# Optimization experiments

Hardware: AMD Instinct MI355X
Metric: run time of the kernel (lower is better)

Reference implementation:

```python
import jax, jax.numpy as jnp
import numpy as np

H = 1024   # hidden_size == memory_size
NH = 4     # num_attention_heads
HD = H // NH
M = 8192   # total memory items
B, S = 4, 2048
EPS = 1e-5


def _ln(x, g, b):
    mu = jnp.mean(x, -1, keepdims=True)
    var = jnp.mean((x - mu) ** 2, -1, keepdims=True)
    return (x - mu) / jnp.sqrt(var + EPS) * g + b


def setup_inputs() -> dict:
    key = jax.random.key(0)
    ks = jax.random.split(key, 16)
    s = 0.02
    return {
        "query_hidden": jax.random.normal(ks[0], (B, S, H), jnp.float32),
        "mem_keys": jax.random.normal(ks[1], (M, H), jnp.float32),
        "importance": jax.random.uniform(ks[2], (M,), jnp.float32),
        "recency": jax.random.uniform(ks[3], (M,), jnp.float32),
        "access_count": jax.random.uniform(ks[4], (M,), jnp.float32),
        "Wq": s * jax.random.normal(ks[5], (H, H), jnp.float32),
        "bq": jnp.zeros((H,), jnp.float32),
        "in_w": s * jax.random.normal(ks[6], (3 * H, H), jnp.float32),
        "in_b": jnp.zeros((3 * H,), jnp.float32),
        "out_w": s * jax.random.normal(ks[7], (H, H), jnp.float32),
        "out_b": jnp.zeros((H,), jnp.float32),
        "gate_w": s * jax.random.normal(ks[8], (H, 2 * H), jnp.float32),
        "gate_b": jnp.zeros((H,), jnp.float32),
        "int_w1": s * jax.random.normal(ks[9], (2 * H, 2 * H), jnp.float32),
        "int_b1": jnp.zeros((2 * H,), jnp.float32),
        "int_ln_g": jnp.ones((2 * H,), jnp.float32),
        "int_ln_b": jnp.zeros((2 * H,), jnp.float32),
        "int_w2": s * jax.random.normal(ks[10], (H, 2 * H), jnp.float32),
        "int_b2": jnp.zeros((H,), jnp.float32),
        "ln1_g": jnp.ones((H,), jnp.float32),
        "ln1_b": jnp.zeros((H,), jnp.float32),
        "ln2_g": jnp.ones((H,), jnp.float32),
        "ln2_b": jnp.zeros((H,), jnp.float32),
        "sel_params": jnp.ones((3,), jnp.float32) / 3.0,
        "top_k": 2048,
    }


def reference(query_hidden, mem_keys, importance, recency, access_count,
              Wq, bq, in_w, in_b, out_w, out_b, gate_w, gate_b,
              int_w1, int_b1, int_ln_g, int_ln_b, int_w2, int_b2,
              ln1_g, ln1_b, ln2_g, ln2_b, sel_params, top_k):
    b, s, _ = query_hidden.shape
    # HTPS selection: softmax-weighted mix of importance / recency / frequency
    w = jax.nn.softmax(sel_params)
    freq = access_count / jnp.max(access_count)
    sel = w[0] * importance + w[1] * recency + w[2] * freq
    _, idx = jax.lax.top_k(sel, top_k)
    mem = mem_keys[idx]                      # [K, H]
    mem_n = _ln(mem, ln1_g, ln1_b)           # layer_norm1 on memory

    q = query_hidden @ Wq.T + bq             # query_proj  [B,S,H]
    wq, wk, wv = in_w[:H], in_w[H:2 * H], in_w[2 * H:]
    bqi, bki, bvi = in_b[:H], in_b[H:2 * H], in_b[2 * H:]
    # Batched MHA: the per-position loop is equivalent to all S queries at once
    Q = (q @ wq.T + bqi).reshape(b, s, NH, HD)
    K = (mem_n @ wk.T + bki).reshape(top_k, NH, HD)   # shared across batch
    V = (mem_n @ wv.T + bvi).reshape(top_k, NH, HD)
    scores = jnp.einsum('bshd,khd->bhsk', Q, K) / jnp.sqrt(jnp.float32(HD))
    attn = jax.nn.softmax(scores, axis=-1)
    ctx = jnp.einsum('bhsk,khd->bshd', attn, V).reshape(b, s, H)
    attn_out = ctx @ out_w.T + out_b

    cat = jnp.concatenate([query_hidden, attn_out], axis=-1)   # [B,S,2H]
    gate = jax.nn.sigmoid(cat @ gate_w.T + gate_b)
    h1 = _ln(cat @ int_w1.T + int_b1, int_ln_g, int_ln_b)
    integ = jax.nn.gelu(h1, approximate=False) @ int_w2.T + int_b2
    return _ln(query_hidden + gate * integ, ln2_g, ln2_b)
```

## Files before the change

kernel.cpp:

```cpp
#include <hip/hip_runtime.h>

#define HDIM 1024
#define MMEM 8192
#define TOPK 2048
#define NROWS 8192
#define LNEPS 1e-5f

typedef unsigned short ushort_t;
typedef __bf16 bf16x8 __attribute__((ext_vector_type(8)));
typedef float f32x4 __attribute__((ext_vector_type(4)));
typedef __attribute__((address_space(1))) const void GVoid;
typedef __attribute__((address_space(3))) void LVoid;

__device__ __forceinline__ ushort_t f2bf(float f) {
    union { float f; unsigned u; } c; c.f = f;
    unsigned r = c.u + 0x7fffu + ((c.u >> 16) & 1u);
    return (ushort_t)(r >> 16);
}
__device__ __forceinline__ float bf2f(ushort_t u) {
    union { unsigned u; float f; } c; c.u = ((unsigned)u) << 16; return c.f;
}
__device__ __forceinline__ float blk_red(float v, int op, float* red) {
    #pragma unroll
    for (int o = 32; o; o >>= 1) {
        float u = __shfl_down(v, o);
        v = op ? fmaxf(v, u) : v + u;
    }
    if ((threadIdx.x & 63) == 0) red[threadIdx.x >> 6] = v;
    __syncthreads();
    float r = op ? fmaxf(fmaxf(red[0], red[1]), fmaxf(red[2], red[3]))
                 : (red[0] + red[1]) + (red[2] + red[3]);
    __syncthreads();
    return r;
}

__global__ __launch_bounds__(256) void sel_prep(const float* __restrict__ sp,
        const float* __restrict__ imp, const float* __restrict__ rec,
        const float* __restrict__ ac, float* __restrict__ sel) {
    __shared__ float red[4];
    float p0 = sp[0], p1 = sp[1], p2 = sp[2];
    float mx = fmaxf(p0, fmaxf(p1, p2));
    float e0 = expf(p0 - mx), e1 = expf(p1 - mx), e2 = expf(p2 - mx);
    float inv = 1.f / (e0 + e1 + e2);
    float w0 = e0 * inv, w1 = e1 * inv, w2 = e2 * inv;
    float m = -1e30f;
    for (int i = threadIdx.x; i < MMEM; i += 256) m = fmaxf(m, ac[i]);
    m = blk_red(m, 1, red);
    float rinv = 1.f / m;
    for (int i = threadIdx.x; i < MMEM; i += 256)
        sel[i] = w0 * imp[i] + w1 * rec[i] + w2 * (ac[i] * rinv);
}

__global__ __launch_bounds__(256) void topk_rank(const float* __restrict__ sel,
                                                 int* __restrict__ idx) {
    __shared__ float s[MMEM];
    __shared__ int pc[256];
    for (int t = threadIdx.x; t < MMEM / 4; t += 256)
        reinterpret_cast<float4*>(s)[t] = reinterpret_cast<const float4*>(sel)[t];
    __syncthreads();
    const int li = threadIdx.x & 31;
    const int jc = threadIdx.x >> 5;
    const int i  = blockIdx.x * 32 + li;
    const float si = s[i];
    int cnt = 0;
    const float4* sv = reinterpret_cast<const float4*>(s) + jc * 256;
    #pragma unroll 4
    for (int t = 0; t < 256; ++t) {
        float4 v = sv[t];
        int j0 = jc * 1024 + t * 4;
        cnt += (v.x > si) || (v.x == si && (j0 + 0) < i);
        cnt += (v.y > si) || (v.y == si && (j0 + 1) < i);
        cnt += (v.z > si) || (v.z == si && (j0 + 2) < i);
        cnt += (v.w > si) || (v.w == si && (j0 + 3) < i);
    }
    pc[threadIdx.x] = cnt;
    __syncthreads();
    if (threadIdx.x < 32) {
        int r = 0;
        #pragma unroll
        for (int c = 0; c < 8; ++c) r += pc[c * 32 + threadIdx.x];
        if (r < TOPK) idx[r] = blockIdx.x * 32 + threadIdx.x;
    }
}

__global__ __launch_bounds__(256) void gather_ln(const float* __restrict__ mem_keys,
        const int* __restrict__ idx, const float* __restrict__ g,
        const float* __restrict__ b, ushort_t* __restrict__ out) {
    __shared__ float red[4];
    int src = idx[blockIdx.x] & (MMEM - 1);
    const float* x = mem_keys + (size_t)src * HDIM;
    float4 v = reinterpret_cast<const float4*>(x)[threadIdx.x];
    float s = v.x + v.y + v.z + v.w;
    float ss = v.x*v.x + v.y*v.y + v.z*v.z + v.w*v.w;
    s  = blk_red(s, 0, red);
    ss = blk_red(ss, 0, red);
    float mu = s * (1.f / HDIM);
    float var = ss * (1.f / HDIM) - mu * mu;
    float rstd = rsqrtf(var + LNEPS);
    int c = threadIdx.x * 4;
    ushort4 o;
    o.x = f2bf((v.x - mu) * rstd * g[c+0] + b[c+0]);
    o.y = f2bf((v.y - mu) * rstd * g[c+1] + b[c+1]);
    o.z = f2bf((v.z - mu) * rstd * g[c+2] + b[c+2]);
    o.w = f2bf((v.w - mu) * rstd * g[c+3] + b[c+3]);
    *reinterpret_cast<ushort4*>(out + (size_t)blockIdx.x * HDIM + c) = o;
}

__global__ __launch_bounds__(256) void cvt_bf16(const float* __restrict__ in,
                                                ushort_t* __restrict__ out) {
    size_t i = ((size_t)blockIdx.x * 256 + threadIdx.x) * 4;
    float4 v = *reinterpret_cast<const float4*>(in + i);
    ushort4 o = { f2bf(v.x), f2bf(v.y), f2bf(v.z), f2bf(v.w) };
    *reinterpret_cast<ushort4*>(out + i) = o;
}

__global__ __launch_bounds__(256) void cvt_t_bf16(const float* __restrict__ in,
                                                  ushort_t* __restrict__ out) {
    __shared__ ushort_t t[64][65];
    const int bx = blockIdx.x * 64, by = blockIdx.y * 64;
    const int r = threadIdx.x >> 4, c4 = (threadIdx.x & 15) << 2;
    #pragma unroll
    for (int rr = 0; rr < 64; rr += 16) {
        float4 v = *reinterpret_cast<const float4*>(in + (size_t)(by + r + rr) * 1024 + bx + c4);
        t[r + rr][c4 + 0] = f2bf(v.x);
        t[r + rr][c4 + 1] = f2bf(v.y);
        t[r + rr][c4 + 2] = f2bf(v.z);
        t[r + rr][c4 + 3] = f2bf(v.w);
    }
    __syncthreads();
    #pragma unroll
    for (int rr = 0; rr < 64; rr += 16) {
        const int i = r + rr;
        ushort4 o = { t[c4 + 0][i], t[c4 + 1][i], t[c4 + 2][i], t[c4 + 3][i] };
        *reinterpret_cast<ushort4*>(out + (size_t)(bx + i) * 1024 + by + c4) = o;
    }
}

__global__ __launch_bounds__(256) void bias_fold(const float* __restrict__ wq,
        const float* __restrict__ bq, const float* __restrict__ bqi,
        float* __restrict__ beff) {
    __shared__ float red[4];
    const float4 wv = reinterpret_cast<const float4*>(wq + (size_t)blockIdx.x * 1024)[threadIdx.x];
    const float4 bv = reinterpret_cast<const float4*>(bq)[threadIdx.x];
    float s = wv.x*bv.x + wv.y*bv.y + wv.z*bv.z + wv.w*bv.w;
    s = blk_red(s, 0, red);
    if (threadIdx.x == 0) beff[blockIdx.x] = s + bqi[blockIdx.x];
}

__global__ __launch_bounds__(256) void cvt_x_cat(const float* __restrict__ x,
                                                 ushort_t* __restrict__ cat) {
    size_t i = ((size_t)blockIdx.x * 256 + threadIdx.x) * 4;
    size_t row = i >> 10, col = i & 1023;
    float4 v = *reinterpret_cast<const float4*>(x + i);
    ushort4 o = { f2bf(v.x), f2bf(v.y), f2bf(v.z), f2bf(v.w) };
    *reinterpret_cast<ushort4*>(cat + row * 2048 + col) = o;
}

__global__ __launch_bounds__(256) void softmax_rows(ushort_t* __restrict__ sc) {
    __shared__ float red[4];
    ushort_t* p = sc + (size_t)blockIdx.x * 2048 + threadIdx.x * 8;
    ushort4 a = reinterpret_cast<const ushort4*>(p)[0];
    ushort4 bq = reinterpret_cast<const ushort4*>(p)[1];
    float v[8] = { bf2f(a.x), bf2f(a.y), bf2f(a.z), bf2f(a.w),
                   bf2f(bq.x), bf2f(bq.y), bf2f(bq.z), bf2f(bq.w) };
    float mx = v[0];
    #pragma unroll
    for (int j = 1; j < 8; ++j) mx = fmaxf(mx, v[j]);
    mx = blk_red(mx, 1, red);
    float s = 0.f;
    #pragma unroll
    for (int j = 0; j < 8; ++j) { v[j] = expf(v[j] - mx); s += v[j]; }
    s = blk_red(s, 0, red);
    float inv = 1.f / s;
    ushort4 o1 = { f2bf(v[0]*inv), f2bf(v[1]*inv), f2bf(v[2]*inv), f2bf(v[3]*inv) };
    ushort4 o2 = { f2bf(v[4]*inv), f2bf(v[5]*inv), f2bf(v[6]*inv), f2bf(v[7]*inv) };
    reinterpret_cast<ushort4*>(p)[0] = o1;
    reinterpret_cast<ushort4*>(p)[1] = o2;
}

__global__ __launch_bounds__(256) void ln_gelu(ushort_t* h1,
        const float* __restrict__ g, const float* __restrict__ b) {
    __shared__ float red[4];
    ushort_t* p = h1 + (size_t)blockIdx.x * 2048 + threadIdx.x * 8;
    ushort4 a = reinterpret_cast<const ushort4*>(p)[0];
    ushort4 c = reinterpret_cast<const ushort4*>(p)[1];
    float v[8] = { bf2f(a.x), bf2f(a.y), bf2f(a.z), bf2f(a.w),
                   bf2f(c.x), bf2f(c.y), bf2f(c.z), bf2f(c.w) };
    float s = 0.f, ss = 0.f;
    #pragma unroll
    for (int j = 0; j < 8; ++j) { s += v[j]; ss += v[j]*v[j]; }
    s  = blk_red(s, 0, red);
    ss = blk_red(ss, 0, red);
    float mu = s * (1.f / 2048.f);
    float var = ss * (1.f / 2048.f) - mu * mu;
    float rstd = rsqrtf(var + LNEPS);
    int c0 = threadIdx.x * 8;
    ushort_t o[8];
    #pragma unroll
    for (int j = 0; j < 8; ++j) {
        float xn = (v[j] - mu) * rstd * g[c0 + j] + b[c0 + j];
        float ge = 0.5f * xn * (1.f + erff(xn * 0.70710678118654752f));
        o[j] = f2bf(ge);
    }
    ushort4 o1 = { o[0], o[1], o[2], o[3] };
    ushort4 o2 = { o[4], o[5], o[6], o[7] };
    reinterpret_cast<ushort4*>(p)[0] = o1;
    reinterpret_cast<ushort4*>(p)[1] = o2;
}

__global__ __launch_bounds__(256) void final_ln(const float* __restrict__ x,
        const float* gate, const ushort_t* __restrict__ integ,
        const float* __restrict__ g, const float* __restrict__ b,
        float* out) {
    __shared__ float red[4];
    size_t base = (size_t)blockIdx.x * HDIM + threadIdx.x * 4;
    float4 xv = *reinterpret_cast<const float4*>(x + base);
    float4 gv = *reinterpret_cast<const float4*>(gate + base);
    ushort4 iv = *reinterpret_cast<const ushort4*>(integ + base);
    float v[4] = { xv.x + gv.x*bf2f(iv.x), xv.y + gv.y*bf2f(iv.y),
                   xv.z + gv.z*bf2f(iv.z), xv.w + gv.w*bf2f(iv.w) };
    float s = v[0]+v[1]+v[2]+v[3];
    float ss = v[0]*v[0]+v[1]*v[1]+v[2]*v[2]+v[3]*v[3];
    s  = blk_red(s, 0, red);
    ss = blk_red(ss, 0, red);
    float mu = s * (1.f / HDIM);
    float var = ss * (1.f / HDIM) - mu * mu;
    float rstd = rsqrtf(var + LNEPS);
    int c = threadIdx.x * 4;
    float4 o;
    o.x = (v[0] - mu) * rstd * g[c+0] + b[c+0];
    o.y = (v[1] - mu) * rstd * g[c+1] + b[c+1];
    o.z = (v[2] - mu) * rstd * g[c+2] + b[c+2];
    o.w = (v[3] - mu) * rstd * g[c+3] + b[c+3];
    *reinterpret_cast<float4*>(out + base) = o;
}

template<int EPI, int BIAS>
__global__ __launch_bounds__(256, 2)
void gemm_bt(const ushort_t* __restrict__ A, const ushort_t* __restrict__ B,
             const float* __restrict__ bias, void* __restrict__ Cv,
             int K, int lda, int ldb, int ldc,
             long long sA1, long long sA2, long long sAz,
             long long sB1, long long sB2, long long sBz,
             long long sC1, long long sC2, long long sCz,
             int z2n, int zbase, float scale)
{
    __shared__ __align__(16) ushort_t As[8192];
    __shared__ __align__(16) ushort_t Bs[8192];
    const int zz = blockIdx.z;
    const int zg = zz + zbase;
    const int z1 = zg / z2n, z2 = zg - z1 * z2n;
    A += (size_t)(z1 * sA1 + z2 * sA2 + zz * sAz);
    B += (size_t)(z1 * sB1 + z2 * sB2 + zz * sBz);
    const size_t cOff = (size_t)(z1 * sC1 + z2 * sC2 + zz * sCz);

    const int nwg = gridDim.x * gridDim.y;
    const int wg  = blockIdx.y * gridDim.x + blockIdx.x;
    const int q8  = nwg >> 3, r8 = nwg & 7;
    const int xcd = wg & 7, lo = wg >> 3;
    const int wgid = (xcd < r8 ? xcd * (q8 + 1) : r8 * (q8 + 1) + (xcd - r8) * q8) + lo;
    const int m0 = (wgid / gridDim.x) * 128, n0 = (wgid % gridDim.x) * 128;

    const int tid = threadIdx.x;
    const int w = tid >> 6, l = tid & 63;
    const int wm = w >> 1, wn = w & 1;

    f32x4 acc[4][4] = {};
    const int srow = l >> 3;
    const int scol = ((l & 7) ^ srow) << 3;

    for (int k0 = 0; k0 < K; k0 += 64) {
        #pragma unroll
        for (int i = 0; i < 4; ++i) {
            const int c = i * 4 + w;
            const int row = c * 8 + srow;
            const ushort_t* ga = A + (size_t)(m0 + row) * lda + (k0 + scol);
            const ushort_t* gb = B + (size_t)(n0 + row) * ldb + (k0 + scol);
            __builtin_amdgcn_global_load_lds((GVoid*)ga, (LVoid*)(As + c * 512), 16, 0, 0);
            __builtin_amdgcn_global_load_lds((GVoid*)gb, (LVoid*)(Bs + c * 512), 16, 0, 0);
        }
        __syncthreads();
        #pragma unroll
        for (int kk = 0; kk < 2; ++kk) {
            bf16x8 af[4], bfv[4];
            #pragma unroll
            for (int m = 0; m < 4; ++m) {
                const int row = wm * 64 + m * 16 + (l & 15);
                const int cb = ((kk * 64) + ((l >> 4) * 16)) ^ ((row & 7) << 4);
                af[m] = *reinterpret_cast<const bf16x8*>(
                    reinterpret_cast<const char*>(As) + row * 128 + cb);
            }
            #pragma unroll
            for (int n = 0; n < 4; ++n) {
                const int row = wn * 64 + n * 16 + (l & 15);
                const int cb = ((kk * 64) + ((l >> 4) * 16)) ^ ((row & 7) << 4);
                bfv[n] = *reinterpret_cast<const bf16x8*>(
                    reinterpret_cast<const char*>(Bs) + row * 128 + cb);
            }
            #pragma unroll
            for (int m = 0; m < 4; ++m)
                #pragma unroll
                for (int n = 0; n < 4; ++n)
                    acc[m][n] = __builtin_amdgcn_mfma_f32_16x16x32_bf16(
                        af[m], bfv[n], acc[m][n], 0, 0, 0);
        }
        __syncthreads();
    }

    #pragma unroll
    for (int m = 0; m < 4; ++m) {
        const int grow = m0 + wm * 64 + m * 16 + ((l >> 4) << 2);
        #pragma unroll
        for (int n = 0; n < 4; ++n) {
            const int gcol = n0 + wn * 64 + n * 16 + (l & 15);
            float bc = (BIAS == 1) ? bias[gcol] : 0.f;
            #pragma unroll
            for (int j = 0; j < 4; ++j) {
                float v = acc[m][n][j] * scale;
                if (BIAS == 1) v += bc;
                if (BIAS == 2) v += bias[grow + j];
                if (EPI == 2) v = 1.f / (1.f + expf(-v));
                const size_t off = cOff + (size_t)(grow + j) * ldc + gcol;
                if (EPI == 1) ((ushort_t*)Cv)[off] = f2bf(v);
                else          ((float*)Cv)[off]    = v;
            }
        }
    }
}

extern "C" void kernel_launch(void* const* d_in, const int* in_sizes, int n_in,
                              void* d_out, int out_size, void* d_ws, size_t ws_size,
                              hipStream_t stream) {
    const float* x          = (const float*)d_in[0];
    const float* mem_keys   = (const float*)d_in[1];
    const float* importance = (const float*)d_in[2];
    const float* recency    = (const float*)d_in[3];
    const float* access_cnt = (const float*)d_in[4];
    const float* Wq         = (const float*)d_in[5];
    const float* bq         = (const float*)d_in[6];
    const float* in_w       = (const float*)d_in[7];
    const float* in_b       = (const float*)d_in[8];
    const float* out_w      = (const float*)d_in[9];
    const float* out_b      = (const float*)d_in[10];
    const float* gate_w     = (const float*)d_in[11];
    const float* gate_b     = (const float*)d_in[12];
    const float* int_w1     = (const float*)d_in[13];
    const float* int_b1     = (const float*)d_in[14];
    const float* int_ln_g   = (const float*)d_in[15];
    const float* int_ln_b   = (const float*)d_in[16];
    const float* int_w2     = (const float*)d_in[17];
    const float* int_b2     = (const float*)d_in[18];
    const float* ln1_g      = (const float*)d_in[19];
    const float* ln1_b      = (const float*)d_in[20];
    const float* ln2_g      = (const float*)d_in[21];
    const float* ln2_b      = (const float*)d_in[22];
    const float* sel_params = (const float*)d_in[23];

    char* ws = (char*)d_ws;
    size_t off = 0;
    auto alloc = [&](size_t bytes) -> char* {
        char* p = ws + off;
        off = (off + bytes + 255) & ~(size_t)255;
        return p;
    };

    float*    sel      = (float*)alloc(MMEM * 4);
    int*      idx      = (int*)alloc(TOPK * 4);
    float*    beff     = (float*)alloc(1024 * 4);
    ushort_t* wqT_bf   = (ushort_t*)alloc((size_t)1048576 * 2);
    ushort_t* weff_bf  = (ushort_t*)alloc((size_t)1048576 * 2);
    ushort_t* inw_bf   = (ushort_t*)alloc((size_t)3145728 * 2);
    ushort_t* outw_bf  = (ushort_t*)alloc((size_t)1048576 * 2);
    ushort_t* gatew_bf = (ushort_t*)alloc((size_t)2097152 * 2);
    ushort_t* intw1_bf = (ushort_t*)alloc((size_t)4194304 * 2);
    ushort_t* intw2_bf = (ushort_t*)alloc((size_t)2097152 * 2);
    ushort_t* mem_n    = (ushort_t*)alloc((size_t)TOPK * HDIM * 2);
    ushort_t* Kbuf     = (ushort_t*)alloc((size_t)TOPK * HDIM * 2);
    ushort_t* Vt       = (ushort_t*)alloc((size_t)HDIM * TOPK * 2);
    ushort_t* cat      = (ushort_t*)alloc((size_t)NROWS * 2048 * 2);
    ushort_t* qQ       = (ushort_t*)alloc((size_t)NROWS * 2048 * 2);
    ushort_t* Qbuf     = qQ + (size_t)NROWS * HDIM;
    ushort_t* h1       = qQ;
    ushort_t* ctx      = (ushort_t*)alloc((size_t)NROWS * HDIM * 2);
    ushort_t* integ    = ctx;
    float*    gatev    = (float*)d_out;

    int NC = 8;
    while (NC > 1 && off + (size_t)NC * 8388608 > ws_size) NC >>= 1;
    ushort_t* scores = (ushort_t*)alloc((size_t)NC * 8388608);

    cvt_t_bf16<<<dim3(16,16), 256, 0, stream>>>(Wq, wqT_bf);
    cvt_bf16<<<3072, 256, 0, stream>>>(in_w, inw_bf);
    cvt_bf16<<<1024, 256, 0, stream>>>(out_w, outw_bf);
    cvt_bf16<<<2048, 256, 0, stream>>>(gate_w, gatew_bf);
    cvt_bf16<<<4096, 256, 0, stream>>>(int_w1, intw1_bf);
    cvt_bf16<<<2048, 256, 0, stream>>>(int_w2, intw2_bf);
    cvt_x_cat<<<8192, 256, 0, stream>>>(x, cat);
    bias_fold<<<1024, 256, 0, stream>>>(in_w, bq, in_b, beff);

    gemm_bt<1,0><<<dim3(8,8,1), 256, 0, stream>>>(inw_bf, wqT_bf, nullptr, weff_bf,
        1024, 1024, 1024, 1024, 0,0,0, 0,0,0, 0,0,0, 1, 0, 1.f);

    sel_prep<<<1, 256, 0, stream>>>(sel_params, importance, recency, access_cnt, sel);
    topk_rank<<<MMEM/32, 256, 0, stream>>>(sel, idx);
    gather_ln<<<TOPK, 256, 0, stream>>>(mem_keys, idx, ln1_g, ln1_b, mem_n);

    gemm_bt<1,1><<<dim3(8,64,1), 256, 0, stream>>>(cat, weff_bf, beff, Qbuf,
        1024, 2048, 1024, 1024, 0,0,0, 0,0,0, 0,0,0, 1, 0, 1.f);
    gemm_bt<1,1><<<dim3(8,16,1), 256, 0, stream>>>(mem_n, inw_bf + 1048576, in_b + 1024,
        Kbuf, 1024, 1024, 1024, 1024, 0,0,0, 0,0,0, 0,0,0, 1, 0, 1.f);
    gemm_bt<1,2><<<dim3(16,8,1), 256, 0, stream>>>(inw_bf + 2097152, mem_n, in_b + 2048,
        Vt, 1024, 1024, 1024, 2048, 0,0,0, 0,0,0, 0,0,0, 1, 0, 1.f);

    for (int c0 = 0; c0 < 16; c0 += NC) {
        gemm_bt<1,0><<<dim3(16,16,NC), 256, 0, stream>>>(Qbuf, Kbuf, nullptr, scores,
            256, 1024, 1024, 2048,
            2097152, 256, 0,  0, 256, 0,  0, 0, 4194304, 4, c0, 0.0625f);
        softmax_rows<<<NC * 2048, 256, 0, stream>>>(scores);
        gemm_bt<1,0><<<dim3(2,16,NC), 256, 0, stream>>>(scores, Vt, nullptr, ctx,
            2048, 2048, 2048, 1024,
            0, 0, 4194304,  0, 524288, 0,  2097152, 256, 0, 4, c0, 1.f);
    }

    gemm_bt<1,1><<<dim3(8,64,1), 256, 0, stream>>>(ctx, outw_bf, out_b,
        (void*)(cat + 1024), 1024, 1024, 1024, 2048, 0,0,0, 0,0,0, 0,0,0, 1, 0, 1.f);

    gemm_bt<2,1><<<dim3(8,64,1), 256, 0, stream>>>(cat, gatew_bf, gate_b, gatev,
        2048, 2048, 2048, 1024, 0,0,0, 0,0,0, 0,0,0, 1, 0, 1.f);
    gemm_bt<1,1><<<dim3(16,64,1), 256, 0, stream>>>(cat, intw1_bf, int_b1, h1,
        2048, 2048, 2048, 2048, 0,0,0, 0,0,0, 0,0,0, 1, 0, 1.f);
    ln_gelu<<<NROWS, 256, 0, stream>>>(h1, int_ln_g, int_ln_b);
    gemm_bt<1,1><<<dim3(8,64,1), 256, 0, stream>>>(h1, intw2_bf, int_b2, integ,
        2048, 2048, 2048, 1024, 0,0,0, 0,0,0, 0,0,0, 1, 0, 1.f);
    final_ln<<<NROWS, 256, 0, stream>>>(x, gatev, integ, ln2_g, ln2_b, (float*)d_out);
}
```

Measured before the change: 594.9 us.

## Fuse gate and int_w1 GEMMs, batch weight conversions, wave-per-row softmax

After: 584.1 us. About the same (-1.8%).

```diff
diff --git a/kernel.cpp b/kernel.cpp
--- a/kernel.cpp
+++ b/kernel.cpp
@@ -106,12 +106,22 @@
     *reinterpret_cast<ushort4*>(out + (size_t)blockIdx.x * HDIM + c) = o;
 }
 
-__global__ __launch_bounds__(256) void cvt_bf16(const float* __restrict__ in,
-                                                ushort_t* __restrict__ out) {
-    size_t i = ((size_t)blockIdx.x * 256 + threadIdx.x) * 4;
-    float4 v = *reinterpret_cast<const float4*>(in + i);
+__global__ __launch_bounds__(256) void cvt_all(const float* __restrict__ in_w,
+        const float* __restrict__ out_w, const float* __restrict__ gate_w,
+        const float* __restrict__ int_w1, const float* __restrict__ int_w2,
+        ushort_t* __restrict__ inw_bf, ushort_t* __restrict__ outw_bf,
+        ushort_t* __restrict__ gw3, ushort_t* __restrict__ intw2_bf) {
+    const int b = blockIdx.x;
+    const float* src; ushort_t* dst; int rel;
+    if      (b < 3072)  { src = in_w;   dst = inw_bf;        rel = b; }
+    else if (b < 4096)  { src = out_w;  dst = outw_bf;       rel = b - 3072; }
+    else if (b < 6144)  { src = gate_w; dst = gw3;           rel = b - 4096; }
+    else if (b < 10240) { src = int_w1; dst = gw3 + 2097152; rel = b - 6144; }
+    else                { src = int_w2; dst = intw2_bf;      rel = b - 10240; }
+    size_t i = ((size_t)rel * 256 + threadIdx.x) * 4;
+    float4 v = *reinterpret_cast<const float4*>(src + i);
     ushort4 o = { f2bf(v.x), f2bf(v.y), f2bf(v.z), f2bf(v.w) };
-    *reinterpret_cast<ushort4*>(out + i) = o;
+    *reinterpret_cast<ushort4*>(dst + i) = o;
 }
 
 __global__ __launch_bounds__(256) void cvt_t_bf16(const float* __restrict__ in,
@@ -157,25 +167,47 @@
 }
 
 __global__ __launch_bounds__(256) void softmax_rows(ushort_t* __restrict__ sc) {
-    __shared__ float red[4];
-    ushort_t* p = sc + (size_t)blockIdx.x * 2048 + threadIdx.x * 8;
-    ushort4 a = reinterpret_cast<const ushort4*>(p)[0];
-    ushort4 bq = reinterpret_cast<const ushort4*>(p)[1];
-    float v[8] = { bf2f(a.x), bf2f(a.y), bf2f(a.z), bf2f(a.w),
-                   bf2f(bq.x), bf2f(bq.y), bf2f(bq.z), bf2f(bq.w) };
+    const int row = blockIdx.x * 4 + (threadIdx.x >> 6);
+    const int l = threadIdx.x & 63;
+    uint4* p = reinterpret_cast<uint4*>(sc + (size_t)row * 2048 + l * 32);
+    uint4 u[4];
+    #pragma unroll
+    for (int i = 0; i < 4; ++i) u[i] = p[i];
+    float v[32];
+    #pragma unroll
+    for (int i = 0; i < 4; ++i) {
+        unsigned* w = reinterpret_cast<unsigned*>(&u[i]);
+        #pragma unroll
+        for (int k = 0; k < 4; ++k) {
+            union { unsigned u; float f; } lo, hi;
+            lo.u = w[k] << 16; hi.u = w[k] & 0xffff0000u;
+            v[i*8 + k*2]     = lo.f;
+            v[i*8 + k*2 + 1] = hi.f;
+        }
+    }
     float mx = v[0];
     #pragma unroll
-    for (int j = 1; j < 8; ++j) mx = fmaxf(mx, v[j]);
-    mx = blk_red(mx, 1, red);
+    for (int j = 1; j < 32; ++j) mx = fmaxf(mx, v[j]);
+    #pragma unroll
+    for (int o = 1; o < 64; o <<= 1) mx = fmaxf(mx, __shfl_xor(mx, o));
     float s = 0.f;
     #pragma unroll
-    for (int j = 0; j < 8; ++j) { v[j] = expf(v[j] - mx); s += v[j]; }
-    s = blk_red(s, 0, red);
+    for (int j = 0; j < 32; ++j) { v[j] = expf(v[j] - mx); s += v[j]; }
+    #pragma unroll
+    for (int o = 1; o < 64; o <<= 1) s += __shfl_xor(s, o);
     float inv = 1.f / s;
-    ushort4 o1 = { f2bf(v[0]*inv), f2bf(v[1]*inv), f2bf(v[2]*inv), f2bf(v[3]*inv) };
-    ushort4 o2 = { f2bf(v[4]*inv), f2bf(v[5]*inv), f2bf(v[6]*inv), f2bf(v[7]*inv) };
-    reinterpret_cast<ushort4*>(p)[0] = o1;
-    reinterpret_cast<ushort4*>(p)[1] = o2;
+    #pragma unroll
+    for (int i = 0; i < 4; ++i) {
+        unsigned* w = reinterpret_cast<unsigned*>(&u[i]);
+        #pragma unroll
+        for (int k = 0; k < 4; ++k) {
+            unsigned lo = f2bf(v[i*8 + k*2] * inv);
+            unsigned hi = f2bf(v[i*8 + k*2 + 1] * inv);
+            w[k] = lo | (hi << 16);
+        }
+    }
+    #pragma unroll
+    for (int i = 0; i < 4; ++i) p[i] = u[i];
 }
 
 __global__ __launch_bounds__(256) void ln_gelu(ushort_t* h1,
@@ -209,16 +241,16 @@
 }
 
 __global__ __launch_bounds__(256) void final_ln(const float* __restrict__ x,
-        const float* gate, const ushort_t* __restrict__ integ,
+        const ushort_t* __restrict__ gate, const ushort_t* __restrict__ integ,
         const float* __restrict__ g, const float* __restrict__ b,
-        float* out) {
+        float* __restrict__ out) {
     __shared__ float red[4];
     size_t base = (size_t)blockIdx.x * HDIM + threadIdx.x * 4;
     float4 xv = *reinterpret_cast<const float4*>(x + base);
-    float4 gv = *reinterpret_cast<const float4*>(gate + base);
+    ushort4 gv = *reinterpret_cast<const ushort4*>(gate + base);
     ushort4 iv = *reinterpret_cast<const ushort4*>(integ + base);
-    float v[4] = { xv.x + gv.x*bf2f(iv.x), xv.y + gv.y*bf2f(iv.y),
-                   xv.z + gv.z*bf2f(iv.z), xv.w + gv.w*bf2f(iv.w) };
+    float v[4] = { xv.x + bf2f(gv.x)*bf2f(iv.x), xv.y + bf2f(gv.y)*bf2f(iv.y),
+                   xv.z + bf2f(gv.z)*bf2f(iv.z), xv.w + bf2f(gv.w)*bf2f(iv.w) };
     float s = v[0]+v[1]+v[2]+v[3];
     float ss = v[0]*v[0]+v[1]*v[1]+v[2]*v[2]+v[3]*v[3];
     s  = blk_red(s, 0, red);
@@ -239,6 +271,7 @@
 __global__ __launch_bounds__(256, 2)
 void gemm_bt(const ushort_t* __restrict__ A, const ushort_t* __restrict__ B,
              const float* __restrict__ bias, void* __restrict__ Cv,
+             void* __restrict__ Cv2, const float* __restrict__ bias2,
              int K, int lda, int ldb, int ldc,
              long long sA1, long long sA2, long long sAz,
              long long sB1, long long sB2, long long sBz,
@@ -316,13 +349,25 @@
             float bc = (BIAS == 1) ? bias[gcol] : 0.f;
             #pragma unroll
             for (int j = 0; j < 4; ++j) {
-                float v = acc[m][n][j] * scale;
-                if (BIAS == 1) v += bc;
-                if (BIAS == 2) v += bias[grow + j];
-                if (EPI == 2) v = 1.f / (1.f + expf(-v));
-                const size_t off = cOff + (size_t)(grow + j) * ldc + gcol;
-                if (EPI == 1) ((ushort_t*)Cv)[off] = f2bf(v);
-                else          ((float*)Cv)[off]    = v;
+                if (EPI == 3) {
+                    float v = acc[m][n][j];
+                    if (gcol < 1024) {
+                        v += bias[gcol];
+                        v = 1.f / (1.f + expf(-v));
+                        ((ushort_t*)Cv)[(size_t)(grow + j) * ldc + gcol] = f2bf(v);
+                    } else {
+                        v += bias2[gcol - 1024];
+                        ((ushort_t*)Cv2)[(size_t)(grow + j) * 2048 + (gcol - 1024)] = f2bf(v);
+                    }
+                } else {
+                    float v = acc[m][n][j] * scale;
+                    if (BIAS == 1) v += bc;
+                    if (BIAS == 2) v += bias[grow + j];
+                    if (EPI == 2) v = 1.f / (1.f + expf(-v));
+                    const size_t off = cOff + (size_t)(grow + j) * ldc + gcol;
+                    if (EPI == 1) ((ushort_t*)Cv)[off] = f2bf(v);
+                    else          ((float*)Cv)[off]    = v;
+                }
             }
         }
     }
@@ -371,8 +416,7 @@
     ushort_t* weff_bf  = (ushort_t*)alloc((size_t)1048576 * 2);
     ushort_t* inw_bf   = (ushort_t*)alloc((size_t)3145728 * 2);
     ushort_t* outw_bf  = (ushort_t*)alloc((size_t)1048576 * 2);
-    ushort_t* gatew_bf = (ushort_t*)alloc((size_t)2097152 * 2);
-    ushort_t* intw1_bf = (ushort_t*)alloc((size_t)4194304 * 2);
+    ushort_t* gw3      = (ushort_t*)alloc((size_t)6291456 * 2);
     ushort_t* intw2_bf = (ushort_t*)alloc((size_t)2097152 * 2);
     ushort_t* mem_n    = (ushort_t*)alloc((size_t)TOPK * HDIM * 2);
     ushort_t* Kbuf     = (ushort_t*)alloc((size_t)TOPK * HDIM * 2);
@@ -383,54 +427,51 @@
     ushort_t* h1       = qQ;
     ushort_t* ctx      = (ushort_t*)alloc((size_t)NROWS * HDIM * 2);
     ushort_t* integ    = ctx;
-    float*    gatev    = (float*)d_out;
-
-    int NC = 8;
+
+    int NC = 16;
     while (NC > 1 && off + (size_t)NC * 8388608 > ws_size) NC >>= 1;
     ushort_t* scores = (ushort_t*)alloc((size_t)NC * 8388608);
+    ushort_t* gatev  = scores;
 
     cvt_t_bf16<<<dim3(16,16), 256, 0, stream>>>(Wq, wqT_bf);
-    cvt_bf16<<<3072, 256, 0, stream>>>(in_w, inw_bf);
-    cvt_bf16<<<1024, 256, 0, stream>>>(out_w, outw_bf);
-    cvt_bf16<<<2048, 256, 0, stream>>>(gate_w, gatew_bf);
-    cvt_bf16<<<4096, 256, 0, stream>>>(int_w1, intw1_bf);
-    cvt_bf16<<<2048, 256, 0, stream>>>(int_w2, intw2_bf);
+    cvt_all<<<12288, 256, 0, stream>>>(in_w, out_w, gate_w, int_w1, int_w2,
+                                       inw_bf, outw_bf, gw3, intw2_bf);
     cvt_x_cat<<<8192, 256, 0, stream>>>(x, cat);
     bias_fold<<<1024, 256, 0, stream>>>(in_w, bq, in_b, beff);
 
     gemm_bt<1,0><<<dim3(8,8,1), 256, 0, stream>>>(inw_bf, wqT_bf, nullptr, weff_bf,
-        1024, 1024, 1024, 1024, 0,0,0, 0,0,0, 0,0,0, 1, 0, 1.f);
+        nullptr, nullptr, 1024, 1024, 1024, 1024, 0,0,0, 0,0,0, 0,0,0, 1, 0, 1.f);
 
     sel_prep<<<1, 256, 0, stream>>>(sel_params, importance, recency, access_cnt, sel);
     topk_rank<<<MMEM/32, 256, 0, stream>>>(sel, idx);
     gather_ln<<<TOPK, 256, 0, stream>>>(mem_keys, idx, ln1_g, ln1_b, mem_n);
 
     gemm_bt<1,1><<<dim3(8,64,1), 256, 0, stream>>>(cat, weff_bf, beff, Qbuf,
-        1024, 2048, 1024, 1024, 0,0,0, 0,0,0, 0,0,0, 1, 0, 1.f);
+        nullptr, nullptr, 1024, 2048, 1024, 1024, 0,0,0, 0,0,0, 0,0,0, 1, 0, 1.f);
     gemm_bt<1,1><<<dim3(8,16,1), 256, 0, stream>>>(mem_n, inw_bf + 1048576, in_b + 1024,
-        Kbuf, 1024, 1024, 1024, 1024, 0,0,0, 0,0,0, 0,0,0, 1, 0, 1.f);
+        Kbuf, nullptr, nullptr, 1024, 1024, 1024, 1024, 0,0,0, 0,0,0, 0,0,0, 1, 0, 1.f);
     gemm_bt<1,2><<<dim3(16,8,1), 256, 0, stream>>>(inw_bf + 2097152, mem_n, in_b + 2048,
-        Vt, 1024, 1024, 1024, 2048, 0,0,0, 0,0,0, 0,0,0, 1, 0, 1.f);
+        Vt, nullptr, nullptr, 1024, 1024, 1024, 2048, 0,0,0, 0,0,0, 0,0,0, 1, 0, 1.f);
 
     for (int c0 = 0; c0 < 16; c0 += NC) {
         gemm_bt<1,0><<<dim3(16,16,NC), 256, 0, stream>>>(Qbuf, Kbuf, nullptr, scores,
-            256, 1024, 1024, 2048,
+            nullptr, nullptr, 256, 1024, 1024, 2048,
             2097152, 256, 0,  0, 256, 0,  0, 0, 4194304, 4, c0, 0.0625f);
-        softmax_rows<<<NC * 2048, 256, 0, stream>>>(scores);
+        softmax_rows<<<NC * 512, 256, 0, stream>>>(scores);
         gemm_bt<1,0><<<dim3(2,16,NC), 256, 0, stream>>>(scores, Vt, nullptr, ctx,
-            2048, 2048, 2048, 1024,
+            nullptr, nullptr, 2048, 2048, 2048, 1024,
             0, 0, 4194304,  0, 524288, 0,  2097152, 256, 0, 4, c0, 1.f);
     }
 
     gemm_bt<1,1><<<dim3(8,64,1), 256, 0, stream>>>(ctx, outw_bf, out_b,
-        (void*)(cat + 1024), 1024, 1024, 1024, 2048, 0,0,0, 0,0,0, 0,0,0, 1, 0, 1.f);
-
-    gemm_bt<2,1><<<dim3(8,64,1), 256, 0, stream>>>(cat, gatew_bf, gate_b, gatev,
-        2048, 2048, 2048, 1024, 0,0,0, 0,0,0, 0,0,0, 1, 0, 1.f);
-    gemm_bt<1,1><<<dim3(16,64,1), 256, 0, stream>>>(cat, intw1_bf, int_b1, h1,
-        2048, 2048, 2048, 2048, 0,0,0, 0,0,0, 0,0,0, 1, 0, 1.f);
+        (void*)(cat + 1024), nullptr, nullptr, 1024, 1024, 1024, 2048,
+        0,0,0, 0,0,0, 0,0,0, 1, 0, 1.f);
+
+    gemm_bt<3,0><<<dim3(24,64,1), 256, 0, stream>>>(cat, gw3, gate_b, gatev,
+        h1, int_b1, 2048, 2048, 2048, 1024, 0,0,0, 0,0,0, 0,0,0, 1, 0, 1.f);
+
     ln_gelu<<<NROWS, 256, 0, stream>>>(h1, int_ln_g, int_ln_b);
     gemm_bt<1,1><<<dim3(8,64,1), 256, 0, stream>>>(h1, intw2_bf, int_b2, integ,
-        2048, 2048, 2048, 1024, 0,0,0, 0,0,0, 0,0,0, 1, 0, 1.f);
+        nullptr, nullptr, 2048, 2048, 2048, 1024, 0,0,0, 0,0,0, 0,0,0, 1, 0, 1.f);
     final_ln<<<NROWS, 256, 0, stream>>>(x, gatev, integ, ln2_g, ln2_b, (float*)d_out);
 }
```
